# Optimization experiments

Hardware: AMD Instinct MI355X
Metric: run time of the kernel (lower is better)

The kernel has to match this reference:

```python
import jax, jax.numpy as jnp
import numpy as np


def setup_inputs() -> dict:
    key = jax.random.key(0)
    B, T, V, H, C = 128, 256, 128, 512, 128  # batch, seq_length, input_dim, num_hidden, num_classes
    ks = jax.random.split(key, 10)

    def xavier(k, shape):
        fan_in, fan_out = shape
        lim = jnp.sqrt(6.0 / (fan_in + fan_out)).astype(jnp.float32)
        return jax.random.uniform(k, shape, jnp.float32, -lim, lim)

    inp = {
        'x': jax.random.randint(ks[0], (B, T), 0, V, dtype=jnp.int32),
        'W_xg': xavier(ks[1], (V, H)), 'W_hg': xavier(ks[2], (H, H)),
        'W_xi': xavier(ks[3], (V, H)), 'W_hi': xavier(ks[4], (H, H)),
        'W_xf': xavier(ks[5], (V, H)), 'W_hf': xavier(ks[6], (H, H)),
        'W_xo': xavier(ks[7], (V, H)), 'W_ho': xavier(ks[8], (H, H)),
        'W_hp': xavier(ks[9], (H, C)),
        'b_g': jnp.zeros((H,), jnp.float32), 'b_i': jnp.zeros((H,), jnp.float32),
        'b_f': jnp.zeros((H,), jnp.float32), 'b_o': jnp.zeros((H,), jnp.float32),
        'b_p': jnp.zeros((C,), jnp.float32),
    }
    return inp


def reference(x, W_xg, W_hg, W_xi, W_hi, W_xf, W_hf, W_xo, W_ho, W_hp,
              b_g, b_i, b_f, b_o, b_p):
    B, T = x.shape
    H = W_hg.shape[0]
    # one-hot(x_t) @ W_x* == row-gather W_x*[x_t]; same math, no dense one-hot.
    xs = x[:, : T - 1].T  # [T-1, B] token ids; loop runs seq_length-1 steps

    def step(carry, idx):
        h, c = carry
        g = jnp.tanh(W_xg[idx] + h @ W_hg + b_g)
        i = jax.nn.sigmoid(W_xi[idx] + h @ W_hi + b_i)
        f = jax.nn.sigmoid(W_xf[idx] + h @ W_hf + b_f)
        o = jax.nn.sigmoid(W_xo[idx] + h @ W_ho + b_o)
        c = g * i + c * f
        h = jnp.tanh(c) * o
        return (h, c), None

    h0 = jnp.zeros((B, H), jnp.float32)
    c0 = jnp.zeros((B, H), jnp.float32)
    (h, _), _ = jax.lax.scan(step, (h0, c0), xs)
    return h @ W_hp + b_p
```

## Files before the change

kernel.cpp:

```cpp
#include <hip/hip_runtime.h>


typedef __attribute__((ext_vector_type(8))) short short8;
typedef __attribute__((ext_vector_type(4))) float f32x4;
typedef __attribute__((ext_vector_type(16))) unsigned int u32x16;

#define NGROUPS 8
#define WGS_PER_GROUP 32
#define HDIM 512
#define TT 256
#define NSTEPS 255
#define CDIM 128
#define PGQ 4096
#define TAGB_OFF 1024

__device__ unsigned long long g_hbuf[4 * NGROUPS * PGQ];
__device__ unsigned int g_sync[TAGB_OFF + NGROUPS * WGS_PER_GROUP * 16];

static __device__ __forceinline__ unsigned short f32_to_bf16(float f) {
  unsigned int u = __builtin_bit_cast(unsigned int, f);
  u += 0x7fffu + ((u >> 16) & 1u);
  return (unsigned short)(u >> 16);
}
static __device__ __forceinline__ float bf16_to_f32(unsigned short s) {
  unsigned int u = ((unsigned int)s) << 16;
  return __builtin_bit_cast(float, u);
}
static __device__ __forceinline__ float fast_sigmoid(float v) {
  return __builtin_amdgcn_rcpf(1.0f + __expf(-v));
}
static __device__ __forceinline__ float fast_tanh(float v) {
  return 1.0f - 2.0f * __builtin_amdgcn_rcpf(1.0f + __expf(2.0f * v));
}

static __device__ __forceinline__ unsigned int poll_min32(const unsigned int* p) {
  u32x16 A, B;
  asm volatile("s_dcache_inv\n\t"
               "s_load_dwordx16 %0, %1, 0x0\n\t"
               "s_waitcnt lgkmcnt(0)"
               : "=&s"(A) : "s"(p) : "memory");
  unsigned int m = A[0];
#pragma unroll
  for (int i = 1; i < 16; ++i) m = (A[i] < m) ? A[i] : m;
  asm volatile("s_load_dwordx16 %0, %1, 0x40\n\t"
               "s_waitcnt lgkmcnt(0)"
               : "=&s"(B) : "s"(p) : "memory");
#pragma unroll
  for (int i = 0; i < 16; ++i) m = (B[i] < m) ? B[i] : m;
  return m;
}

static __device__ __forceinline__ void wait_group(const unsigned int* tagA,
                                                  const unsigned int* tagBlane,
                                                  unsigned int tgt) {
  for (int spins = 0; spins < 256; ++spins) {
    if (poll_min32(tagA) >= tgt) return;
  }
  for (;;) {
    const unsigned int v = __hip_atomic_load(tagBlane, __ATOMIC_RELAXED,
                                             __HIP_MEMORY_SCOPE_AGENT);
    if (__all((int)(v >= tgt))) return;
    __builtin_amdgcn_s_sleep(1);
  }
}

__global__ __launch_bounds__(256, 1) void lstm_persistent(
    const int* __restrict__ x,
    const float* __restrict__ Wxg, const float* __restrict__ Whg,
    const float* __restrict__ Wxi, const float* __restrict__ Whi,
    const float* __restrict__ Wxf, const float* __restrict__ Whf,
    const float* __restrict__ Wxo, const float* __restrict__ Who,
    const float* __restrict__ Whp,
    const float* __restrict__ bg, const float* __restrict__ bi,
    const float* __restrict__ bf, const float* __restrict__ bo,
    const float* __restrict__ bp,
    float* __restrict__ out)
{
  const int bid = blockIdx.x;
  const int g = bid & 7;
  const int w = bid >> 3;
  const int tid = threadIdx.x;
  const int wave = tid >> 6;
  const int lane = tid & 63;
  const int lane15 = lane & 15;
  const int lanehi = lane >> 4;

  __shared__ float part[2][4][4][16][20];
  __shared__ int lds_x[16][TT];
  __shared__ unsigned int lds_ctr;

  if (tid == 0) lds_ctr = 0u;
  for (int i = tid; i < 16 * TT; i += 256)
    ((int*)lds_x)[i] = x[g * 16 * TT + i];

  const float* Whs[4] = {Whg, Whi, Whf, Who};
  const int bcol = (w << 4) + lane15;
  short8 wf[4][4][2];
#pragma unroll
  for (int gate = 0; gate < 4; ++gate) {
    const float* Wh = Whs[gate];
#pragma unroll
    for (int ksl = 0; ksl < 4; ++ksl) {
      const int ksg = (wave << 2) + ksl;
      short8 s0, s1;
#pragma unroll
      for (int e = 0; e < 8; ++e) {
        float v = Wh[(ksg * 32 + lanehi * 8 + e) * HDIM + bcol];
        unsigned short a = f32_to_bf16(v);
        unsigned short b = f32_to_bf16(v - bf16_to_f32(a));
        s0[e] = (short)a; s1[e] = (short)b;
      }
      wf[gate][ksl][0] = s0; wf[gate][ksl][1] = s1;
    }
  }
  __syncthreads();

  const int brow = tid >> 4;
  const int jl = tid & 15;
  const int j = (w << 4) + jl;
  const float bgv = bg[j], biv = bi[j], bfv = bf[j], bov = bo[j];
  const int pidx = ((j >> 5) << 8) + ((((j >> 3) & 3) << 4) + brow) * 4 + ((j & 7) >> 1);

  const unsigned int* tagA = g_sync + (g << 5);
  const unsigned int* tagBlane =
      g_sync + TAGB_OFF + ((unsigned)(g * 32 + (lane & 31)) << 4);
  unsigned int* myA = g_sync + (g << 5) + w;
  unsigned int* myB = g_sync + TAGB_OFF + ((unsigned)(g * 32 + w) << 4);

  float creg = 0.0f;

  for (int t = 0; t < NSTEPS; ++t) {
    const int idx = lds_x[brow][t];
    const float xgv = Wxg[idx * HDIM + j];
    const float xiv = Wxi[idx * HDIM + j];
    const float xfv = Wxf[idx * HDIM + j];
    const float xov = Wxo[idx * HDIM + j];

    f32x4 acc[4] = {{0.f,0.f,0.f,0.f},{0.f,0.f,0.f,0.f},
                    {0.f,0.f,0.f,0.f},{0.f,0.f,0.f,0.f}};
    if (t > 0) {
      wait_group(tagA, tagBlane, (unsigned int)t);
      const unsigned long long* srcq =
          g_hbuf + ((size_t)((t & 3) * NGROUPS + g)) * PGQ;
      unsigned long long q[16];
#pragma unroll
      for (int ksl = 0; ksl < 4; ++ksl) {
        const int base = ((wave << 2) + ksl) * 256 + (lane << 2);
#pragma unroll
        for (int u = 0; u < 4; ++u)
          q[ksl * 4 + u] = srcq[base + u];
      }
#pragma unroll
      for (int ksl = 0; ksl < 4; ++ksl) {
        unsigned int lo[4], hi[4];
#pragma unroll
        for (int u = 0; u < 4; ++u) {
          lo[u] = (unsigned int)q[ksl * 4 + u];
          hi[u] = (unsigned int)(q[ksl * 4 + u] >> 32);
        }
        short8 a0, a1;
#pragma unroll
        for (int u = 0; u < 4; ++u) {
          a0[2*u] = (short)(lo[u] & 0xffffu); a0[2*u+1] = (short)(lo[u] >> 16);
          a1[2*u] = (short)(hi[u] & 0xffffu); a1[2*u+1] = (short)(hi[u] >> 16);
        }
#pragma unroll
        for (int gate = 0; gate < 4; ++gate) {
          acc[gate] = __builtin_amdgcn_mfma_f32_16x16x32_bf16(a0, wf[gate][ksl][0], acc[gate], 0, 0, 0);
          acc[gate] = __builtin_amdgcn_mfma_f32_16x16x32_bf16(a0, wf[gate][ksl][1], acc[gate], 0, 0, 0);
          acc[gate] = __builtin_amdgcn_mfma_f32_16x16x32_bf16(a1, wf[gate][ksl][0], acc[gate], 0, 0, 0);
        }
      }
    }
    {
      const int crow = lanehi << 2;
      const int pb = t & 1;
#pragma unroll
      for (int gate = 0; gate < 4; ++gate)
        *(f32x4*)&part[pb][wave][gate][lane15][crow] = acc[gate];
    }
    __syncthreads();

    const int pb = t & 1;
    const float pg = part[pb][0][0][jl][brow] + part[pb][1][0][jl][brow] +
                     part[pb][2][0][jl][brow] + part[pb][3][0][jl][brow] + xgv + bgv;
    const float pi = part[pb][0][1][jl][brow] + part[pb][1][1][jl][brow] +
                     part[pb][2][1][jl][brow] + part[pb][3][1][jl][brow] + xiv + biv;
    const float pf = part[pb][0][2][jl][brow] + part[pb][1][2][jl][brow] +
                     part[pb][2][2][jl][brow] + part[pb][3][2][jl][brow] + xfv + bfv;
    const float po = part[pb][0][3][jl][brow] + part[pb][1][3][jl][brow] +
                     part[pb][2][3][jl][brow] + part[pb][3][3][jl][brow] + xov + bov;
    const float gv = fast_tanh(pg);
    const float iv = fast_sigmoid(pi);
    const float fv = fast_sigmoid(pf);
    const float ov = fast_sigmoid(po);
    creg = gv * iv + creg * fv;
    const float hv = fast_tanh(creg) * ov;

    const unsigned short h0 = f32_to_bf16(hv);
    const unsigned short h1 = f32_to_bf16(hv - bf16_to_f32(h0));
    const unsigned int pa = (unsigned int)h0 | ((unsigned int)h1 << 16);
    const unsigned int na = (unsigned int)__shfl_xor((int)pa, 1);
    if (!(jl & 1)) {
      unsigned long long* dstq =
          g_hbuf + ((size_t)(((t + 1) & 3) * NGROUPS + g)) * PGQ;
      const unsigned int w0 = (pa & 0xffffu) | ((na & 0xffffu) << 16);
      const unsigned int w1 = (pa >> 16) | (na & 0xffff0000u);
      dstq[pidx] = (unsigned long long)w0 | ((unsigned long long)w1 << 32);
    }
    asm volatile("s_waitcnt vmcnt(0)" ::: "memory");
    if (lane == 0) {
      const unsigned int old = atomicAdd(&lds_ctr, 1u);
      if ((old & 3u) == 3u) {
        __hip_atomic_store(myA, (unsigned int)(t + 1), __ATOMIC_RELAXED,
                           __HIP_MEMORY_SCOPE_WORKGROUP);
        __hip_atomic_store(myB, (unsigned int)(t + 1), __ATOMIC_RELAXED,
                           __HIP_MEMORY_SCOPE_AGENT);
      }
    }
  }

  wait_group(tagA, tagBlane, (unsigned int)NSTEPS);
  __syncthreads();
  {
    const unsigned long long* srcq =
        g_hbuf + ((size_t)((NSTEPS & 3) * NGROUPS + g)) * PGQ;
    const int bq = tid >> 4;
    const int q15 = tid & 15;
    const int cloc = q15 >> 2;
    const int ksl2 = q15 & 3;
    const int cc = (w << 2) + cloc;
    float sum = 0.0f;
    for (int k = ksl2 * 128; k < ksl2 * 128 + 128; k += 2) {
      const int pk = ((k >> 5) << 8) + ((((k >> 3) & 3) << 4) + bq) * 4 + ((k & 7) >> 1);
      const unsigned long long qv = srcq[pk];
      const unsigned int w0 = (unsigned int)qv;
      const unsigned int w1 = (unsigned int)(qv >> 32);
      const float hk0 = bf16_to_f32((unsigned short)(w0 & 0xffffu)) +
                        bf16_to_f32((unsigned short)(w1 & 0xffffu));
      const float hk1 = bf16_to_f32((unsigned short)(w0 >> 16)) +
                        bf16_to_f32((unsigned short)(w1 >> 16));
      sum += hk0 * Whp[k * CDIM + cc] + hk1 * Whp[(k + 1) * CDIM + cc];
    }
    float* gb = &part[0][0][0][0][0];
    gb[tid] = sum;
    __syncthreads();
    if (ksl2 == 0) {
      const float res = gb[tid] + gb[tid + 1] + gb[tid + 2] + gb[tid + 3] + bp[cc];
      out[(g * 16 + bq) * CDIM + cc] = res;
    }
  }
}

extern "C" void kernel_launch(void* const* d_in, const int* in_sizes, int n_in,
                              void* d_out, int out_size, void* d_ws, size_t ws_size,
                              hipStream_t stream) {
  (void)in_sizes; (void)n_in; (void)out_size; (void)d_ws; (void)ws_size;
  const int* x = (const int*)d_in[0];
  const float* Wxg = (const float*)d_in[1];
  const float* Whg = (const float*)d_in[2];
  const float* Wxi = (const float*)d_in[3];
  const float* Whi = (const float*)d_in[4];
  const float* Wxf = (const float*)d_in[5];
  const float* Whf = (const float*)d_in[6];
  const float* Wxo = (const float*)d_in[7];
  const float* Who = (const float*)d_in[8];
  const float* Whp = (const float*)d_in[9];
  const float* bg = (const float*)d_in[10];
  const float* bi = (const float*)d_in[11];
  const float* bf = (const float*)d_in[12];
  const float* bo = (const float*)d_in[13];
  const float* bp = (const float*)d_in[14];
  float* out = (float*)d_out;

  void* sync_dev = nullptr;
  hipGetSymbolAddress(&sync_dev, HIP_SYMBOL(g_sync));
  hipMemsetAsync(sync_dev, 0,
                 sizeof(unsigned int) * (TAGB_OFF + NGROUPS * WGS_PER_GROUP * 16),
                 stream);

  lstm_persistent<<<dim3(256), dim3(256), 0, stream>>>(
      x, Wxg, Whg, Wxi, Whi, Wxf, Whf, Wxo, Who, Whp,
      bg, bi, bf, bo, bp, out);
}
```

Measured before the change: 497.9 us.

## Wait only on the eight producer workgroups each wave actually reads

Each wave now polls only the 8 workgroup tags that produce its K-slice of h, not all 32 in the group, using a single scalar dwordx8 load. The tag pointers are forced into SGPRs, the spin limit before falling back to the sleep loop is raised, the bf16 operand packing becomes a bit_cast, and the LDS partial-sum layout is transposed to remove padding. The intent is to shorten the per-step barrier latency on the serial recurrence. The risk is heavier spinning on the scalar cache and possible LDS bank conflicts from the new layout.

```diff
diff --git a/kernel.cpp b/kernel.cpp
--- a/kernel.cpp
+++ b/kernel.cpp
@@ -3,6 +3,8 @@
 
 typedef __attribute__((ext_vector_type(8))) short short8;
 typedef __attribute__((ext_vector_type(4))) float f32x4;
+typedef __attribute__((ext_vector_type(4))) unsigned int u32x4;
+typedef __attribute__((ext_vector_type(8))) unsigned int u32x8;
 typedef __attribute__((ext_vector_type(16))) unsigned int u32x16;
 
 #define NGROUPS 8
@@ -32,7 +34,24 @@
 static __device__ __forceinline__ float fast_tanh(float v) {
   return 1.0f - 2.0f * __builtin_amdgcn_rcpf(1.0f + __expf(2.0f * v));
 }
-
+static __device__ __forceinline__ const unsigned int* sgpr_ptr(const unsigned int* p) {
+  const unsigned long long u = (unsigned long long)p;
+  const unsigned int lo = __builtin_amdgcn_readfirstlane((unsigned int)u);
+  const unsigned int hi = __builtin_amdgcn_readfirstlane((unsigned int)(u >> 32));
+  return (const unsigned int*)(((unsigned long long)hi << 32) | (unsigned long long)lo);
+}
+
+static __device__ __forceinline__ unsigned int poll_min8(const unsigned int* p) {
+  u32x8 A;
+  asm volatile("s_dcache_inv\n\t"
+               "s_load_dwordx8 %0, %1, 0x0\n\t"
+               "s_waitcnt lgkmcnt(0)"
+               : "=&s"(A) : "s"(p) : "memory");
+  unsigned int m = A[0];
+#pragma unroll
+  for (int i = 1; i < 8; ++i) m = (A[i] < m) ? A[i] : m;
+  return m;
+}
 static __device__ __forceinline__ unsigned int poll_min32(const unsigned int* p) {
   u32x16 A, B;
   asm volatile("s_dcache_inv\n\t"
@@ -50,10 +69,23 @@
   return m;
 }
 
-static __device__ __forceinline__ void wait_group(const unsigned int* tagA,
+static __device__ __forceinline__ void wait_prod8(const unsigned int* tag8,
                                                   const unsigned int* tagBlane,
                                                   unsigned int tgt) {
-  for (int spins = 0; spins < 256; ++spins) {
+  for (int spins = 0; spins < 4096; ++spins) {
+    if (poll_min8(tag8) >= tgt) return;
+  }
+  for (;;) {
+    const unsigned int v = __hip_atomic_load(tagBlane, __ATOMIC_RELAXED,
+                                             __HIP_MEMORY_SCOPE_AGENT);
+    if (__all((int)(v >= tgt))) return;
+    __builtin_amdgcn_s_sleep(1);
+  }
+}
+static __device__ __forceinline__ void wait_group32(const unsigned int* tagA,
+                                                    const unsigned int* tagBlane,
+                                                    unsigned int tgt) {
+  for (int spins = 0; spins < 4096; ++spins) {
     if (poll_min32(tagA) >= tgt) return;
   }
   for (;;) {
@@ -85,7 +117,7 @@
   const int lane15 = lane & 15;
   const int lanehi = lane >> 4;
 
-  __shared__ float part[2][4][4][16][20];
+  __shared__ float part[2][4][4][16][16];
   __shared__ int lds_x[16][TT];
   __shared__ unsigned int lds_ctr;
 
@@ -121,7 +153,8 @@
   const float bgv = bg[j], biv = bi[j], bfv = bf[j], bov = bo[j];
   const int pidx = ((j >> 5) << 8) + ((((j >> 3) & 3) << 4) + brow) * 4 + ((j & 7) >> 1);
 
-  const unsigned int* tagA = g_sync + (g << 5);
+  const unsigned int* tagA = sgpr_ptr(g_sync + (g << 5));
+  const unsigned int* tag8 = sgpr_ptr(g_sync + (g << 5) + (wave << 3));
   const unsigned int* tagBlane =
       g_sync + TAGB_OFF + ((unsigned)(g * 32 + (lane & 31)) << 4);
   unsigned int* myA = g_sync + (g << 5) + w;
@@ -139,7 +172,7 @@
     f32x4 acc[4] = {{0.f,0.f,0.f,0.f},{0.f,0.f,0.f,0.f},
                     {0.f,0.f,0.f,0.f},{0.f,0.f,0.f,0.f}};
     if (t > 0) {
-      wait_group(tagA, tagBlane, (unsigned int)t);
+      wait_prod8(tag8, tagBlane, (unsigned int)t);
       const unsigned long long* srcq =
           g_hbuf + ((size_t)((t & 3) * NGROUPS + g)) * PGQ;
       unsigned long long q[16];
@@ -152,18 +185,14 @@
       }
 #pragma unroll
       for (int ksl = 0; ksl < 4; ++ksl) {
-        unsigned int lo[4], hi[4];
+        u32x4 lo, hi;
 #pragma unroll
         for (int u = 0; u < 4; ++u) {
           lo[u] = (unsigned int)q[ksl * 4 + u];
           hi[u] = (unsigned int)(q[ksl * 4 + u] >> 32);
         }
-        short8 a0, a1;
-#pragma unroll
-        for (int u = 0; u < 4; ++u) {
-          a0[2*u] = (short)(lo[u] & 0xffffu); a0[2*u+1] = (short)(lo[u] >> 16);
-          a1[2*u] = (short)(hi[u] & 0xffffu); a1[2*u+1] = (short)(hi[u] >> 16);
-        }
+        const short8 a0 = __builtin_bit_cast(short8, lo);
+        const short8 a1 = __builtin_bit_cast(short8, hi);
 #pragma unroll
         for (int gate = 0; gate < 4; ++gate) {
           acc[gate] = __builtin_amdgcn_mfma_f32_16x16x32_bf16(a0, wf[gate][ksl][0], acc[gate], 0, 0, 0);
@@ -177,19 +206,21 @@
       const int pb = t & 1;
 #pragma unroll
       for (int gate = 0; gate < 4; ++gate)
-        *(f32x4*)&part[pb][wave][gate][lane15][crow] = acc[gate];
+#pragma unroll
+        for (int r = 0; r < 4; ++r)
+          part[pb][wave][gate][crow + r][lane15] = acc[gate][r];
     }
     __syncthreads();
 
     const int pb = t & 1;
-    const float pg = part[pb][0][0][jl][brow] + part[pb][1][0][jl][brow] +
-                     part[pb][2][0][jl][brow] + part[pb][3][0][jl][brow] + xgv + bgv;
-    const float pi = part[pb][0][1][jl][brow] + part[pb][1][1][jl][brow] +
-                     part[pb][2][1][jl][brow] + part[pb][3][1][jl][brow] + xiv + biv;
-    const float pf = part[pb][0][2][jl][brow] + part[pb][1][2][jl][brow] +
-                     part[pb][2][2][jl][brow] + part[pb][3][2][jl][brow] + xfv + bfv;
-    const float po = part[pb][0][3][jl][brow] + part[pb][1][3][jl][brow] +
-                     part[pb][2][3][jl][brow] + part[pb][3][3][jl][brow] + xov + bov;
+    const float pg = part[pb][0][0][brow][jl] + part[pb][1][0][brow][jl] +
+                     part[pb][2][0][brow][jl] + part[pb][3][0][brow][jl] + xgv + bgv;
+    const float pi = part[pb][0][1][brow][jl] + part[pb][1][1][brow][jl] +
+                     part[pb][2][1][brow][jl] + part[pb][3][1][brow][jl] + xiv + biv;
+    const float pf = part[pb][0][2][brow][jl] + part[pb][1][2][brow][jl] +
+                     part[pb][2][2][brow][jl] + part[pb][3][2][brow][jl] + xfv + bfv;
+    const float po = part[pb][0][3][brow][jl] + part[pb][1][3][brow][jl] +
+                     part[pb][2][3][brow][jl] + part[pb][3][3][brow][jl] + xov + bov;
     const float gv = fast_tanh(pg);
     const float iv = fast_sigmoid(pi);
     const float fv = fast_sigmoid(pf);
@@ -220,7 +251,7 @@
     }
   }
 
-  wait_group(tagA, tagBlane, (unsigned int)NSTEPS);
+  wait_group32(tagA, tagBlane, (unsigned int)NSTEPS);
   __syncthreads();
   {
     const unsigned long long* srcq =
```

Measured after the change: 417.4 us. 16.2% less time.

## Replace tag-counter barriers with flag bits embedded in the h payload

Applied to the files above, without the earlier changes.

Removes the separate per-workgroup tag counters and the group-wide polling barrier. Each step now writes 2-bit step-phase flags into the low mantissa bits of the bf16 residual halves of h, and consumers poll the h buffer directly until every word carries the expected phase. This drops the vmcnt wait, the LDS atomic and the tag stores from the critical path, and lets a consumer start as soon as its own data has landed. It also splits the MFMA accumulators into two chains and repacks the LDS partials so the reduction reads one vector per wave. The costs are a slight loss of precision in the residual bits, a bounded spin that gives up after a fixed number of sweeps, and a full memset of the h buffer before each launch.

```diff
diff --git a/kernel.cpp b/kernel.cpp
--- a/kernel.cpp
+++ b/kernel.cpp
@@ -3,19 +3,16 @@
 
 typedef __attribute__((ext_vector_type(8))) short short8;
 typedef __attribute__((ext_vector_type(4))) float f32x4;
-typedef __attribute__((ext_vector_type(16))) unsigned int u32x16;
+typedef __attribute__((ext_vector_type(4))) unsigned int u32x4;
 
 #define NGROUPS 8
-#define WGS_PER_GROUP 32
 #define HDIM 512
 #define TT 256
 #define NSTEPS 255
 #define CDIM 128
 #define PGQ 4096
-#define TAGB_OFF 1024
 
 __device__ unsigned long long g_hbuf[4 * NGROUPS * PGQ];
-__device__ unsigned int g_sync[TAGB_OFF + NGROUPS * WGS_PER_GROUP * 16];
 
 static __device__ __forceinline__ unsigned short f32_to_bf16(float f) {
   unsigned int u = __builtin_bit_cast(unsigned int, f);
@@ -32,36 +29,12 @@
 static __device__ __forceinline__ float fast_tanh(float v) {
   return 1.0f - 2.0f * __builtin_amdgcn_rcpf(1.0f + __expf(2.0f * v));
 }
-
-static __device__ __forceinline__ unsigned int poll_min32(const unsigned int* p) {
-  u32x16 A, B;
-  asm volatile("s_dcache_inv\n\t"
-               "s_load_dwordx16 %0, %1, 0x0\n\t"
-               "s_waitcnt lgkmcnt(0)"
-               : "=&s"(A) : "s"(p) : "memory");
-  unsigned int m = A[0];
-#pragma unroll
-  for (int i = 1; i < 16; ++i) m = (A[i] < m) ? A[i] : m;
-  asm volatile("s_load_dwordx16 %0, %1, 0x40\n\t"
-               "s_waitcnt lgkmcnt(0)"
-               : "=&s"(B) : "s"(p) : "memory");
-#pragma unroll
-  for (int i = 0; i < 16; ++i) m = (B[i] < m) ? B[i] : m;
-  return m;
-}
-
-static __device__ __forceinline__ void wait_group(const unsigned int* tagA,
-                                                  const unsigned int* tagBlane,
-                                                  unsigned int tgt) {
-  for (int spins = 0; spins < 256; ++spins) {
-    if (poll_min32(tagA) >= tgt) return;
-  }
-  for (;;) {
-    const unsigned int v = __hip_atomic_load(tagBlane, __ATOMIC_RELAXED,
-                                             __HIP_MEMORY_SCOPE_AGENT);
-    if (__all((int)(v >= tgt))) return;
-    __builtin_amdgcn_s_sleep(1);
-  }
+static __device__ __forceinline__ unsigned long long ag_ld64(const unsigned long long* p) {
+  return __hip_atomic_load(p, __ATOMIC_RELAXED, __HIP_MEMORY_SCOPE_AGENT);
+}
+static __device__ __forceinline__ unsigned int fbits(int s) {
+  const unsigned int F = (unsigned int)(((s >> 2) + 1) & 3);
+  return (F & 1u) | ((F >> 1) << 16);
 }
 
 __global__ __launch_bounds__(256, 1) void lstm_persistent(
@@ -85,11 +58,9 @@
   const int lane15 = lane & 15;
   const int lanehi = lane >> 4;
 
-  __shared__ float part[2][4][4][16][20];
+  __shared__ __align__(16) float part[2][4][16][16][4];
   __shared__ int lds_x[16][TT];
-  __shared__ unsigned int lds_ctr;
-
-  if (tid == 0) lds_ctr = 0u;
+
   for (int i = tid; i < 16 * TT; i += 256)
     ((int*)lds_x)[i] = x[g * 16 * TT + i];
 
@@ -120,12 +91,6 @@
   const int j = (w << 4) + jl;
   const float bgv = bg[j], biv = bi[j], bfv = bf[j], bov = bo[j];
   const int pidx = ((j >> 5) << 8) + ((((j >> 3) & 3) << 4) + brow) * 4 + ((j & 7) >> 1);
-
-  const unsigned int* tagA = g_sync + (g << 5);
-  const unsigned int* tagBlane =
-      g_sync + TAGB_OFF + ((unsigned)(g * 32 + (lane & 31)) << 4);
-  unsigned int* myA = g_sync + (g << 5) + w;
-  unsigned int* myB = g_sync + TAGB_OFF + ((unsigned)(g * 32 + w) << 4);
 
   float creg = 0.0f;
 
@@ -136,60 +101,99 @@
     const float xfv = Wxf[idx * HDIM + j];
     const float xov = Wxo[idx * HDIM + j];
 
-    f32x4 acc[4] = {{0.f,0.f,0.f,0.f},{0.f,0.f,0.f,0.f},
-                    {0.f,0.f,0.f,0.f},{0.f,0.f,0.f,0.f}};
+    f32x4 accA[4] = {{0.f,0.f,0.f,0.f},{0.f,0.f,0.f,0.f},
+                     {0.f,0.f,0.f,0.f},{0.f,0.f,0.f,0.f}};
+    f32x4 accB[4] = {{0.f,0.f,0.f,0.f},{0.f,0.f,0.f,0.f},
+                     {0.f,0.f,0.f,0.f},{0.f,0.f,0.f,0.f}};
     if (t > 0) {
-      wait_group(tagA, tagBlane, (unsigned int)t);
-      const unsigned long long* srcq =
+      const unsigned int expw = fbits(t);
+      const unsigned long long* p0q =
           g_hbuf + ((size_t)((t & 3) * NGROUPS + g)) * PGQ;
-      unsigned long long q[16];
+      u32x4 qa[8];
+
 #pragma unroll
       for (int ksl = 0; ksl < 4; ++ksl) {
         const int base = ((wave << 2) + ksl) * 256 + (lane << 2);
-#pragma unroll
-        for (int u = 0; u < 4; ++u)
-          q[ksl * 4 + u] = srcq[base + u];
-      }
+        qa[ksl * 2]     = *(const u32x4*)(p0q + base);
+        qa[ksl * 2 + 1] = *(const u32x4*)(p0q + base + 2);
+      }
+      int ok = 1;
+#pragma unroll
+      for (int i = 0; i < 8; ++i)
+        ok &= (((qa[i][1] ^ expw) & 0x00010001u) == 0u) &
+              (((qa[i][3] ^ expw) & 0x00010001u) == 0u);
+
+      unsigned int sweeps = 0;
+      while (!__all(ok)) {
+        __builtin_amdgcn_s_sleep(1);
+#pragma unroll
+        for (int ksl = 0; ksl < 4; ++ksl) {
+          const int base = ((wave << 2) + ksl) * 256 + (lane << 2);
+#pragma unroll
+          for (int u = 0; u < 2; ++u) {
+            const unsigned long long v0 = ag_ld64(p0q + base + 2 * u);
+            const unsigned long long v1 = ag_ld64(p0q + base + 2 * u + 1);
+            qa[ksl * 2 + u][0] = (unsigned int)v0;
+            qa[ksl * 2 + u][1] = (unsigned int)(v0 >> 32);
+            qa[ksl * 2 + u][2] = (unsigned int)v1;
+            qa[ksl * 2 + u][3] = (unsigned int)(v1 >> 32);
+          }
+        }
+        ok = 1;
+#pragma unroll
+        for (int i = 0; i < 8; ++i)
+          ok &= (((qa[i][1] ^ expw) & 0x00010001u) == 0u) &
+                (((qa[i][3] ^ expw) & 0x00010001u) == 0u);
+        if (++sweeps > 65536u) break;
+      }
+
 #pragma unroll
       for (int ksl = 0; ksl < 4; ++ksl) {
-        unsigned int lo[4], hi[4];
-#pragma unroll
-        for (int u = 0; u < 4; ++u) {
-          lo[u] = (unsigned int)q[ksl * 4 + u];
-          hi[u] = (unsigned int)(q[ksl * 4 + u] >> 32);
+        const u32x4 A = qa[ksl * 2], B = qa[ksl * 2 + 1];
+        const short8 a0 = __builtin_bit_cast(short8, (u32x4){A[0], A[2], B[0], B[2]});
+        const short8 a1 = __builtin_bit_cast(short8, (u32x4){A[1], A[3], B[1], B[3]});
+        if (ksl < 2) {
+#pragma unroll
+          for (int gate = 0; gate < 4; ++gate) {
+            accA[gate] = __builtin_amdgcn_mfma_f32_16x16x32_bf16(a0, wf[gate][ksl][0], accA[gate], 0, 0, 0);
+            accA[gate] = __builtin_amdgcn_mfma_f32_16x16x32_bf16(a0, wf[gate][ksl][1], accA[gate], 0, 0, 0);
+            accA[gate] = __builtin_amdgcn_mfma_f32_16x16x32_bf16(a1, wf[gate][ksl][0], accA[gate], 0, 0, 0);
+          }
+        } else {
+#pragma unroll
+          for (int gate = 0; gate < 4; ++gate) {
+            accB[gate] = __builtin_amdgcn_mfma_f32_16x16x32_bf16(a0, wf[gate][ksl][0], accB[gate], 0, 0, 0);
+            accB[gate] = __builtin_amdgcn_mfma_f32_16x16x32_bf16(a0, wf[gate][ksl][1], accB[gate], 0, 0, 0);
+            accB[gate] = __builtin_amdgcn_mfma_f32_16x16x32_bf16(a1, wf[gate][ksl][0], accB[gate], 0, 0, 0);
+          }
         }
-        short8 a0, a1;
-#pragma unroll
-        for (int u = 0; u < 4; ++u) {
-          a0[2*u] = (short)(lo[u] & 0xffffu); a0[2*u+1] = (short)(lo[u] >> 16);
-          a1[2*u] = (short)(hi[u] & 0xffffu); a1[2*u+1] = (short)(hi[u] >> 16);
-        }
-#pragma unroll
-        for (int gate = 0; gate < 4; ++gate) {
-          acc[gate] = __builtin_amdgcn_mfma_f32_16x16x32_bf16(a0, wf[gate][ksl][0], acc[gate], 0, 0, 0);
-          acc[gate] = __builtin_amdgcn_mfma_f32_16x16x32_bf16(a0, wf[gate][ksl][1], acc[gate], 0, 0, 0);
-          acc[gate] = __builtin_amdgcn_mfma_f32_16x16x32_bf16(a1, wf[gate][ksl][0], acc[gate], 0, 0, 0);
-        }
-      }
-    }
+      }
+    }
+
     {
       const int crow = lanehi << 2;
       const int pb = t & 1;
 #pragma unroll
-      for (int gate = 0; gate < 4; ++gate)
-        *(f32x4*)&part[pb][wave][gate][lane15][crow] = acc[gate];
+      for (int r = 0; r < 4; ++r) {
+        f32x4 vr;
+#pragma unroll
+        for (int gate = 0; gate < 4; ++gate)
+          vr[gate] = accA[gate][r] + accB[gate][r];
+        *(f32x4*)&part[pb][wave][crow + r][lane15][0] = vr;
+      }
     }
     __syncthreads();
 
     const int pb = t & 1;
-    const float pg = part[pb][0][0][jl][brow] + part[pb][1][0][jl][brow] +
-                     part[pb][2][0][jl][brow] + part[pb][3][0][jl][brow] + xgv + bgv;
-    const float pi = part[pb][0][1][jl][brow] + part[pb][1][1][jl][brow] +
-                     part[pb][2][1][jl][brow] + part[pb][3][1][jl][brow] + xiv + biv;
-    const float pf = part[pb][0][2][jl][brow] + part[pb][1][2][jl][brow] +
-                     part[pb][2][2][jl][brow] + part[pb][3][2][jl][brow] + xfv + bfv;
-    const float po = part[pb][0][3][jl][brow] + part[pb][1][3][jl][brow] +
-                     part[pb][2][3][jl][brow] + part[pb][3][3][jl][brow] + xov + bov;
+    const f32x4 s0 = *(const f32x4*)&part[pb][0][brow][jl][0];
+    const f32x4 s1 = *(const f32x4*)&part[pb][1][brow][jl][0];
+    const f32x4 s2 = *(const f32x4*)&part[pb][2][brow][jl][0];
+    const f32x4 s3 = *(const f32x4*)&part[pb][3][brow][jl][0];
+    const f32x4 pre = s0 + s1 + s2 + s3;
+    const float pg = pre[0] + xgv + bgv;
+    const float pi = pre[1] + xiv + biv;
+    const float pf = pre[2] + xfv + bfv;
+    const float po = pre[3] + xov + bov;
     const float gv = fast_tanh(pg);
     const float iv = fast_sigmoid(pi);
     const float fv = fast_sigmoid(pf);
@@ -205,22 +209,12 @@
       unsigned long long* dstq =
           g_hbuf + ((size_t)(((t + 1) & 3) * NGROUPS + g)) * PGQ;
       const unsigned int w0 = (pa & 0xffffu) | ((na & 0xffffu) << 16);
-      const unsigned int w1 = (pa >> 16) | (na & 0xffff0000u);
+      unsigned int w1 = (pa >> 16) | (na & 0xffff0000u);
+      w1 = (w1 & ~0x00010001u) | fbits(t + 1);
       dstq[pidx] = (unsigned long long)w0 | ((unsigned long long)w1 << 32);
     }
-    asm volatile("s_waitcnt vmcnt(0)" ::: "memory");
-    if (lane == 0) {
-      const unsigned int old = atomicAdd(&lds_ctr, 1u);
-      if ((old & 3u) == 3u) {
-        __hip_atomic_store(myA, (unsigned int)(t + 1), __ATOMIC_RELAXED,
-                           __HIP_MEMORY_SCOPE_WORKGROUP);
-        __hip_atomic_store(myB, (unsigned int)(t + 1), __ATOMIC_RELAXED,
-                           __HIP_MEMORY_SCOPE_AGENT);
-      }
-    }
   }
 
-  wait_group(tagA, tagBlane, (unsigned int)NSTEPS);
   __syncthreads();
   {
     const unsigned long long* srcq =
@@ -230,10 +224,20 @@
     const int cloc = q15 >> 2;
     const int ksl2 = q15 & 3;
     const int cc = (w << 2) + cloc;
+    const unsigned long long expq =
+        (unsigned long long)fbits(NSTEPS) << 32;
     float sum = 0.0f;
     for (int k = ksl2 * 128; k < ksl2 * 128 + 128; k += 2) {
       const int pk = ((k >> 5) << 8) + ((((k >> 3) & 3) << 4) + bq) * 4 + ((k & 7) >> 1);
-      const unsigned long long qv = srcq[pk];
+      unsigned long long qv = srcq[pk];
+      if (((qv >> 32) & 0x00010001ull) != (expq >> 32)) {
+        unsigned int tries = 0;
+        do {
+          __builtin_amdgcn_s_sleep(1);
+          qv = ag_ld64(srcq + pk);
+        } while (((qv >> 32) & 0x00010001ull) != (expq >> 32) &&
+                 ++tries < 65536u);
+      }
       const unsigned int w0 = (unsigned int)qv;
       const unsigned int w1 = (unsigned int)(qv >> 32);
       const float hk0 = bf16_to_f32((unsigned short)(w0 & 0xffffu)) +
@@ -273,11 +277,9 @@
   const float* bp = (const float*)d_in[14];
   float* out = (float*)d_out;
 
-  void* sync_dev = nullptr;
-  hipGetSymbolAddress(&sync_dev, HIP_SYMBOL(g_sync));
-  hipMemsetAsync(sync_dev, 0,
-                 sizeof(unsigned int) * (TAGB_OFF + NGROUPS * WGS_PER_GROUP * 16),
-                 stream);
+  void* hbuf_dev = nullptr;
+  hipGetSymbolAddress(&hbuf_dev, HIP_SYMBOL(g_hbuf));
+  hipMemsetAsync(hbuf_dev, 0, sizeof(g_hbuf), stream);
 
   lstm_persistent<<<dim3(256), dim3(256), 0, stream>>>(
       x, Wxg, Whg, Wxi, Whi, Wxf, Whf, Wxo, Who, Whp,
```

Result: slower. 587.5 us (+18.0%).
